# Performance work log

Measured on AMD Instinct MI355X. Metric: run time of the kernel, lower is better.

## Reference

```python
import jax, jax.numpy as jnp
import numpy as np
import math

EMBED = 512
HEADS = 2
HEAD_DIM = EMBED // HEADS
EPS = 1e-5

def layer_norm(x, g, b):
    mu = jnp.mean(x, axis=-1, keepdims=True)
    var = jnp.var(x, axis=-1, keepdims=True)
    return (x - mu) * jax.lax.rsqrt(var + EPS) * g + b

def setup_inputs() -> dict:
    key = jax.random.key(0)
    ks = jax.random.split(key, 16)
    s = 0.02
    inp = {
        "text_embeds": jax.random.normal(ks[0], (128, 32, EMBED), jnp.float32),
        "video_embeds": jax.random.normal(ks[1], (64, 12, EMBED), jnp.float32),
        "ln1_g": jnp.ones((EMBED,), jnp.float32),
        "ln1_b": jnp.zeros((EMBED,), jnp.float32),
        "Wq": jax.random.normal(ks[2], (EMBED, EMBED), jnp.float32) * s,
        "bq": jnp.zeros((EMBED,), jnp.float32),
        "Wk": jax.random.normal(ks[3], (EMBED, EMBED), jnp.float32) * s,
        "bk": jnp.zeros((EMBED,), jnp.float32),
        "Wv": jax.random.normal(ks[4], (EMBED, EMBED), jnp.float32) * s,
        "bv": jnp.zeros((EMBED,), jnp.float32),
        "Wo": jax.random.normal(ks[5], (EMBED, EMBED), jnp.float32) * s,
        "bo": jnp.zeros((EMBED,), jnp.float32),
        "Wl": jax.random.normal(ks[6], (EMBED, EMBED), jnp.float32) * s,
        "bl": jnp.zeros((EMBED,), jnp.float32),
        "ln2_g": jnp.ones((EMBED,), jnp.float32),
        "ln2_b": jnp.zeros((EMBED,), jnp.float32),
        "ln3_g": jnp.ones((EMBED,), jnp.float32),
        "ln3_b": jnp.zeros((EMBED,), jnp.float32),
    }
    return inp

def reference(text_embeds, video_embeds, ln1_g, ln1_b, Wq, bq, Wk, bk, Wv, bv,
              Wo, bo, Wl, bl, ln2_g, ln2_b, ln3_g, ln3_b):
    # shared layer_norm1 on both modalities
    t = layer_norm(text_embeds, ln1_g, ln1_b)    # [T, Nw, E]
    vd = layer_norm(video_embeds, ln1_g, ln1_b)  # [V, F, E]
    T, Nw, _ = t.shape
    V, Fr, _ = vd.shape
    q = (t @ Wq.T + bq).reshape(T, Nw, HEADS, HEAD_DIM)   # bthd
    k = (vd @ Wk.T + bk).reshape(V, Fr, HEADS, HEAD_DIM)  # avhd
    v = (vd @ Wv.T + bv).reshape(V, Fr, HEADS, HEAD_DIM)  # avhd
    # cross-modal outer-product attention logits: [V, T, H, F, Nw]
    logits = jnp.einsum('avhd,bthd->abhvt', k, q) / math.sqrt(HEAD_DIM)
    weights = jax.nn.softmax(logits, axis=3)  # softmax over frames
    attn = jnp.einsum('avhd,abhvt->abhtd', v, weights)  # [V, T, H, Nw, D]
    attn = attn.transpose(0, 1, 3, 2, 4).reshape(V, T, Nw, EMBED)
    attn = attn.mean(axis=0)                    # [T, Nw, E]
    o = attn @ Wo.T + bo
    o = layer_norm(o, ln2_g, ln2_b)
    lin = o @ Wl.T + bl  # dropout is identity in eval mode
    out = layer_norm(o + lin, ln3_g, ln3_b)
    return out
```

## Files before the change

kernel.cpp:

```cpp
#include <hip/hip_runtime.h>
#include <math.h>

#define EMBED 512
#define HD 256
#define FR 12
#define NV 64
#define NT_TOK 4096
#define NV_TOK 768

typedef __attribute__((ext_vector_type(8))) short short8;
typedef __attribute__((ext_vector_type(4))) float f32x4;

__device__ __forceinline__ unsigned int f2bf(float f) {
  unsigned int u = __float_as_uint(f);
  u += 0x7FFFu + ((u >> 16) & 1u);
  return u >> 16;
}
__device__ __forceinline__ void async_cp16(void* lds, const void* g) {
  __builtin_amdgcn_global_load_lds(
      (const __attribute__((address_space(1))) void*)g,
      (__attribute__((address_space(3))) void*)lds, 16, 0, 0);
}

__device__ __forceinline__ void gemm64_core(
    const unsigned short* __restrict__ Ab, int lda,
    const unsigned short* __restrict__ Bb, int ldb,
    int m0, int n0, int K,
    unsigned short* __restrict__ As, unsigned short* __restrict__ Bs,
    f32x4 acc[2][2]) {
  int tid = threadIdx.x;
  int w = tid >> 6, lane = tid & 63;
  int lr = lane & 15, quad = lane >> 4;
  int wm = (w >> 1) * 32, wn = (w & 1) * 32;
  int rowS[2], cgS[2];
  #pragma unroll
  for (int i = 0; i < 2; ++i) {
    int s = tid + i * 256;
    rowS[i] = s >> 3; cgS[i] = (s & 7) ^ (rowS[i] & 7);
  }
  int nk = K >> 6;
  #pragma unroll
  for (int i = 0; i < 2; ++i) {
    async_cp16(&As[(tid + i * 256) * 8],
               Ab + (size_t)(m0 + rowS[i]) * lda + cgS[i] * 8);
    async_cp16(&Bs[(tid + i * 256) * 8],
               Bb + (size_t)(n0 + rowS[i]) * ldb + cgS[i] * 8);
  }
  for (int k = 0; k < nk; ++k) {
    int cur = k & 1;
    __syncthreads();
    if (k + 1 < nk) {
      int nxt = cur ^ 1, koff = (k + 1) << 6;
      #pragma unroll
      for (int i = 0; i < 2; ++i) {
        async_cp16(&As[nxt * 4096 + (tid + i * 256) * 8],
                   Ab + (size_t)(m0 + rowS[i]) * lda + koff + cgS[i] * 8);
        async_cp16(&Bs[nxt * 4096 + (tid + i * 256) * 8],
                   Bb + (size_t)(n0 + rowS[i]) * ldb + koff + cgS[i] * 8);
      }
    }
    const unsigned short* Ac = As + cur * 4096;
    const unsigned short* Bc = Bs + cur * 4096;
    #pragma unroll
    for (int kk = 0; kk < 2; ++kk) {
      int sw = ((kk * 4 + quad) ^ (lr & 7)) * 8;
      short8 a0 = *(const short8*)&Ac[(wm + lr) * 64 + sw];
      short8 a1 = *(const short8*)&Ac[(wm + 16 + lr) * 64 + sw];
      short8 b0 = *(const short8*)&Bc[(wn + lr) * 64 + sw];
      short8 b1 = *(const short8*)&Bc[(wn + 16 + lr) * 64 + sw];
      acc[0][0] = __builtin_amdgcn_mfma_f32_16x16x32_bf16(a0, b0, acc[0][0], 0, 0, 0);
      acc[0][1] = __builtin_amdgcn_mfma_f32_16x16x32_bf16(a0, b1, acc[0][1], 0, 0, 0);
      acc[1][0] = __builtin_amdgcn_mfma_f32_16x16x32_bf16(a1, b0, acc[1][0], 0, 0, 0);
      acc[1][1] = __builtin_amdgcn_mfma_f32_16x16x32_bf16(a1, b1, acc[1][1], 0, 0, 0);
    }
  }
}

template <int MODE, bool BIAS>
__global__ __launch_bounds__(256, 4) void gemm64(
    const unsigned short* __restrict__ A, int lda, long AzS,
    const unsigned short* __restrict__ B, int ldb, long BzS,
    const float* __restrict__ bias, void* __restrict__ Cv, int ldc, long CzS,
    int K) {
  __shared__ __align__(16) unsigned short As[2 * 4096];
  __shared__ __align__(16) unsigned short Bs[2 * 4096];
  f32x4 acc[2][2] = {};
  const unsigned short* Ab = A + (size_t)blockIdx.z * AzS;
  const unsigned short* Bb = B + (size_t)blockIdx.z * BzS;
  int m0 = blockIdx.x * 64, n0 = blockIdx.y * 64;
  gemm64_core(Ab, lda, Bb, ldb, m0, n0, K, As, Bs, acc);
  int w = threadIdx.x >> 6, lane = threadIdx.x & 63;
  int lr = lane & 15, quad = lane >> 4;
  int wm = (w >> 1) * 32, wn = (w & 1) * 32;
  long cz = (long)blockIdx.z * CzS;
  #pragma unroll
  for (int j = 0; j < 2; ++j) {
    int col = n0 + wn + j * 16 + lr;
    float bv = BIAS ? bias[col] : 0.0f;
    #pragma unroll
    for (int i = 0; i < 2; ++i) {
      int rbase = m0 + wm + i * 16 + quad * 4;
      #pragma unroll
      for (int r = 0; r < 4; ++r) {
        float v = acc[i][j][r] + bv;
        if (MODE == 0)
          ((unsigned short*)Cv)[cz + (size_t)(rbase + r) * ldc + col] =
              (unsigned short)f2bf(v);
        else
          ((float*)Cv)[cz + (size_t)(rbase + r) * ldc + col] = v;
      }
    }
  }
}

__global__ __launch_bounds__(256, 4) void qkv_kernel(
    const unsigned short* __restrict__ tn, const unsigned short* __restrict__ vn,
    const unsigned short* __restrict__ Wq, const unsigned short* __restrict__ Wk,
    const unsigned short* __restrict__ Wv,
    const float* __restrict__ bq, const float* __restrict__ bk,
    const float* __restrict__ bv,
    unsigned short* __restrict__ Q, unsigned short* __restrict__ Kout,
    unsigned short* __restrict__ Vt) {
  __shared__ __align__(16) unsigned short As[2 * 4096];
  __shared__ __align__(16) unsigned short Bs[2 * 4096];
  int bid = blockIdx.x;
  const unsigned short *Ap, *Bp;
  const float* bias;
  unsigned short* outp = nullptr;
  int m0, n0, mode;
  if (bid < 512) {
    Ap = tn; Bp = Wq; bias = bq; outp = Q;
    m0 = (bid >> 3) * 64; n0 = (bid & 7) * 64; mode = 0;
  } else if (bid < 608) {
    int i = bid - 512;
    Ap = vn; Bp = Wk; bias = bk; outp = Kout;
    m0 = (i >> 3) * 64; n0 = (i & 7) * 64; mode = 0;
  } else {
    int i = bid - 608;
    Ap = vn; Bp = Wv; bias = bv;
    m0 = (i >> 3) * 64; n0 = (i & 7) * 64; mode = 1;
  }
  f32x4 acc[2][2] = {};
  gemm64_core(Ap, EMBED, Bp, EMBED, m0, n0, EMBED, As, Bs, acc);
  int w = threadIdx.x >> 6, lane = threadIdx.x & 63;
  int lr = lane & 15, quad = lane >> 4;
  int wm = (w >> 1) * 32, wn = (w & 1) * 32;
  #pragma unroll
  for (int j = 0; j < 2; ++j) {
    int col = n0 + wn + j * 16 + lr;
    float bvv = bias[col];
    #pragma unroll
    for (int i = 0; i < 2; ++i) {
      int rbase = m0 + wm + i * 16 + quad * 4;
      if (mode == 0) {
        #pragma unroll
        for (int r = 0; r < 4; ++r)
          outp[(size_t)(rbase + r) * EMBED + col] =
              (unsigned short)f2bf(acc[i][j][r] + bvv);
      } else {
        ushort4 pk;
        pk.x = (unsigned short)f2bf(acc[i][j][0] + bvv);
        pk.y = (unsigned short)f2bf(acc[i][j][1] + bvv);
        pk.z = (unsigned short)f2bf(acc[i][j][2] + bvv);
        pk.w = (unsigned short)f2bf(acc[i][j][3] + bvv);
        *(ushort4*)&Vt[(size_t)col * NV_TOK + rbase] = pk;
      }
    }
  }
}

__global__ __launch_bounds__(256, 4) void sgemm_softmax(
    const unsigned short* __restrict__ Q, const unsigned short* __restrict__ Kb,
    unsigned short* __restrict__ P) {
  __shared__ __align__(16) char smem[40960];
  unsigned short* As = (unsigned short*)smem;
  unsigned short* Bs = (unsigned short*)(smem + 16384);
  int tid = threadIdx.x;
  int w = tid >> 6, lane = tid & 63;
  int lr = lane & 15, quad = lane >> 4;
  int wm = (w >> 1) * 32, wn = (w & 1) * 48;
  int h = blockIdx.z;
  int m0 = blockIdx.x * 64, n0 = blockIdx.y * 96;
  const unsigned short* Ab = Q + h * HD;
  const unsigned short* Bb = Kb + h * HD;
  int rowA[2], cgA[2], rowB[3], cgB[3];
  #pragma unroll
  for (int i = 0; i < 2; ++i) {
    int s = tid + i * 256;
    rowA[i] = s >> 3; cgA[i] = (s & 7) ^ (rowA[i] & 7);
  }
  #pragma unroll
  for (int i = 0; i < 3; ++i) {
    int s = tid + i * 256;
    rowB[i] = s >> 3; cgB[i] = (s & 7) ^ (rowB[i] & 7);
  }
  f32x4 acc[2][3] = {};
  const int nk = HD >> 6;
  #pragma unroll
  for (int i = 0; i < 2; ++i)
    async_cp16(&As[(tid + i * 256) * 8],
               Ab + (size_t)(m0 + rowA[i]) * EMBED + cgA[i] * 8);
  #pragma unroll
  for (int i = 0; i < 3; ++i)
    async_cp16(&Bs[(tid + i * 256) * 8],
               Bb + (size_t)(n0 + rowB[i]) * EMBED + cgB[i] * 8);
  for (int k = 0; k < nk; ++k) {
    int cur = k & 1;
    __syncthreads();
    if (k + 1 < nk) {
      int nxt = cur ^ 1, koff = (k + 1) << 6;
      #pragma unroll
      for (int i = 0; i < 2; ++i)
        async_cp16(&As[nxt * 4096 + (tid + i * 256) * 8],
                   Ab + (size_t)(m0 + rowA[i]) * EMBED + koff + cgA[i] * 8);
      #pragma unroll
      for (int i = 0; i < 3; ++i)
        async_cp16(&Bs[nxt * 6144 + (tid + i * 256) * 8],
                   Bb + (size_t)(n0 + rowB[i]) * EMBED + koff + cgB[i] * 8);
    }
    const unsigned short* Ac = As + cur * 4096;
    const unsigned short* Bc = Bs + cur * 6144;
    #pragma unroll
    for (int kk = 0; kk < 2; ++kk) {
      int sw = ((kk * 4 + quad) ^ (lr & 7)) * 8;
      short8 a0 = *(const short8*)&Ac[(wm + lr) * 64 + sw];
      short8 a1 = *(const short8*)&Ac[(wm + 16 + lr) * 64 + sw];
      short8 b0 = *(const short8*)&Bc[(wn + lr) * 64 + sw];
      short8 b1 = *(const short8*)&Bc[(wn + 16 + lr) * 64 + sw];
      short8 b2 = *(const short8*)&Bc[(wn + 32 + lr) * 64 + sw];
      acc[0][0] = __builtin_amdgcn_mfma_f32_16x16x32_bf16(a0, b0, acc[0][0], 0, 0, 0);
      acc[0][1] = __builtin_amdgcn_mfma_f32_16x16x32_bf16(a0, b1, acc[0][1], 0, 0, 0);
      acc[0][2] = __builtin_amdgcn_mfma_f32_16x16x32_bf16(a0, b2, acc[0][2], 0, 0, 0);
      acc[1][0] = __builtin_amdgcn_mfma_f32_16x16x32_bf16(a1, b0, acc[1][0], 0, 0, 0);
      acc[1][1] = __builtin_amdgcn_mfma_f32_16x16x32_bf16(a1, b1, acc[1][1], 0, 0, 0);
      acc[1][2] = __builtin_amdgcn_mfma_f32_16x16x32_bf16(a1, b2, acc[1][2], 0, 0, 0);
    }
  }
  __syncthreads();
  float* Sx = (float*)smem;
  #pragma unroll
  for (int j = 0; j < 3; ++j) {
    int col = wn + j * 16 + lr;
    #pragma unroll
    for (int i = 0; i < 2; ++i) {
      int rbase = wm + i * 16 + quad * 4;
      #pragma unroll
      for (int r = 0; r < 4; ++r) Sx[(rbase + r) * 100 + col] = acc[i][j][r];
    }
  }
  __syncthreads();
  unsigned short* Ph = P + (size_t)h * NT_TOK * NV_TOK;
  #pragma unroll
  for (int gi = 0; gi < 2; ++gi) {
    int g = tid * 2 + gi;
    int row = g >> 3, gr = g & 7;
    const float* sp = Sx + row * 100 + gr * 12;
    float v[12];
    float m = -1e30f;
    #pragma unroll
    for (int f = 0; f < FR; ++f) { v[f] = sp[f] * 0.0625f; m = fmaxf(m, v[f]); }
    float s = 0.f;
    #pragma unroll
    for (int f = 0; f < FR; ++f) { v[f] = __expf(v[f] - m); s += v[f]; }
    float inv = (1.0f / NV) / s;
    unsigned short* pp = Ph + (size_t)(m0 + row) * NV_TOK + n0 + gr * 12;
    #pragma unroll
    for (int ii = 0; ii < 6; ++ii) {
      unsigned int lo = f2bf(v[2 * ii] * inv), hi = f2bf(v[2 * ii + 1] * inv);
      *(unsigned int*)(pp + 2 * ii) = lo | (hi << 16);
    }
  }
}

__device__ __forceinline__ void ln_row(
    const float* __restrict__ xr, const float* __restrict__ rr,
    const float* __restrict__ g, const float* __restrict__ b,
    float* __restrict__ outf, unsigned short* __restrict__ outb) {
  int t = threadIdx.x;
  float v0 = xr[t], v1 = xr[t + 256];
  if (rr != nullptr) { v0 += rr[t]; v1 += rr[t + 256]; }
  float s = v0 + v1;
  float s2 = v0 * v0 + v1 * v1;
  #pragma unroll
  for (int off = 32; off > 0; off >>= 1) {
    s += __shfl_down(s, off, 64);
    s2 += __shfl_down(s2, off, 64);
  }
  __shared__ float ss[4], ss2[4];
  __shared__ float mean_s, rstd_s;
  int wid = t >> 6;
  if ((t & 63) == 0) { ss[wid] = s; ss2[wid] = s2; }
  __syncthreads();
  if (t == 0) {
    float a = ss[0] + ss[1] + ss[2] + ss[3];
    float a2 = ss2[0] + ss2[1] + ss2[2] + ss2[3];
    float mean = a * (1.0f / EMBED);
    float var = a2 * (1.0f / EMBED) - mean * mean;
    mean_s = mean;
    rstd_s = rsqrtf(var + 1e-5f);
  }
  __syncthreads();
  float mean = mean_s, rstd = rstd_s;
  float y0 = (v0 - mean) * rstd * g[t] + b[t];
  float y1 = (v1 - mean) * rstd * g[t + 256] + b[t + 256];
  if (outf != nullptr) { outf[t] = y0; outf[t + 256] = y1; }
  if (outb != nullptr) {
    outb[t] = (unsigned short)f2bf(y0);
    outb[t + 256] = (unsigned short)f2bf(y1);
  }
}

__global__ __launch_bounds__(256) void ln_kernel(
    const float* __restrict__ x, const float* __restrict__ res,
    const float* __restrict__ g, const float* __restrict__ b,
    float* __restrict__ outf, unsigned short* __restrict__ outb) {
  size_t row = blockIdx.x;
  ln_row(x + row * EMBED, res ? res + row * EMBED : nullptr, g, b,
         outf ? outf + row * EMBED : nullptr,
         outb ? outb + row * EMBED : nullptr);
}

__global__ __launch_bounds__(256) void prep_kernel(
    const float* __restrict__ text, const float* __restrict__ video,
    const float* __restrict__ g, const float* __restrict__ b,
    const float* __restrict__ Wq, const float* __restrict__ Wk,
    const float* __restrict__ Wv, const float* __restrict__ Wo,
    const float* __restrict__ Wl, unsigned short* __restrict__ Wbf,
    unsigned short* __restrict__ tn, unsigned short* __restrict__ vn) {
  int bid = blockIdx.x;
  if (bid < 1280) {
    int i = bid * 256 + threadIdx.x;
    const float* srcs[5] = {Wq, Wk, Wv, Wo, Wl};
    const float* src = srcs[i >> 16];
    float4 v = ((const float4*)src)[i & 65535];
    uint2 o;
    o.x = f2bf(v.x) | (f2bf(v.y) << 16);
    o.y = f2bf(v.z) | (f2bf(v.w) << 16);
    ((uint2*)Wbf)[i] = o;
    return;
  }
  if (bid < 1280 + NT_TOK) {
    size_t row = bid - 1280;
    ln_row(text + row * EMBED, nullptr, g, b, nullptr, tn + row * EMBED);
  } else {
    size_t row = bid - (1280 + NT_TOK);
    ln_row(video + row * EMBED, nullptr, g, b, nullptr, vn + row * EMBED);
  }
}

extern "C" void kernel_launch(void* const* d_in, const int* in_sizes, int n_in,
                              void* d_out, int out_size, void* d_ws, size_t ws_size,
                              hipStream_t stream) {
  (void)in_sizes; (void)n_in; (void)out_size; (void)ws_size;
  const float* text  = (const float*)d_in[0];
  const float* video = (const float*)d_in[1];
  const float* ln1_g = (const float*)d_in[2];
  const float* ln1_b = (const float*)d_in[3];
  const float* Wq = (const float*)d_in[4];
  const float* bq = (const float*)d_in[5];
  const float* Wk = (const float*)d_in[6];
  const float* bk = (const float*)d_in[7];
  const float* Wv = (const float*)d_in[8];
  const float* bv = (const float*)d_in[9];
  const float* Wo = (const float*)d_in[10];
  const float* bo = (const float*)d_in[11];
  const float* Wl = (const float*)d_in[12];
  const float* bl = (const float*)d_in[13];
  const float* ln2_g = (const float*)d_in[14];
  const float* ln2_b = (const float*)d_in[15];
  const float* ln3_g = (const float*)d_in[16];
  const float* ln3_b = (const float*)d_in[17];
  float* out = (float*)d_out;

  char* base = (char*)d_ws;
  unsigned short* Wbf   = (unsigned short*)base;
  unsigned short* Wq_bf = Wbf + 0 * 262144;
  unsigned short* Wk_bf = Wbf + 1 * 262144;
  unsigned short* Wv_bf = Wbf + 2 * 262144;
  unsigned short* Wo_bf = Wbf + 3 * 262144;
  unsigned short* Wl_bf = Wbf + 4 * 262144;
  unsigned short* Vt    = (unsigned short*)(base + 2621440);
  char* big = base + 3407872;
  unsigned short* Q_bf  = (unsigned short*)(big + 0);
  unsigned short* K_bf  = (unsigned short*)(big + 4194304);
  unsigned short* P     = (unsigned short*)(big + 4980736);
  unsigned short* tn_bf = (unsigned short*)(big + 17563648);
  unsigned short* vn_bf = (unsigned short*)(big + 21757952);
  unsigned short* att_bf = tn_bf;
  float* Ob  = (float*)(big + 4980736);
  float* o2f = (float*)(big + 13369344);
  unsigned short* o2_bf = vn_bf;
  float* lin = (float*)(big + 0);

  prep_kernel<<<1280 + NT_TOK + NV_TOK, 256, 0, stream>>>(
      text, video, ln1_g, ln1_b, Wq, Wk, Wv, Wo, Wl, Wbf, tn_bf, vn_bf);

  qkv_kernel<<<704, 256, 0, stream>>>(tn_bf, vn_bf, Wq_bf, Wk_bf, Wv_bf,
                                      bq, bk, bv, Q_bf, K_bf, Vt);

  sgemm_softmax<<<dim3(64, 8, 2), 256, 0, stream>>>(Q_bf, K_bf, P);

  gemm64<0, false><<<dim3(64, 4, 2), 256, 0, stream>>>(
      P, NV_TOK, (long)NT_TOK * NV_TOK, Vt, NV_TOK, (long)HD * NV_TOK, nullptr,
      att_bf, EMBED, HD, NV_TOK);

  gemm64<1, true><<<dim3(64, 8, 1), 256, 0, stream>>>(
      att_bf, EMBED, 0, Wo_bf, EMBED, 0, bo, Ob, EMBED, 0, EMBED);
  ln_kernel<<<NT_TOK, 256, 0, stream>>>(Ob, nullptr, ln2_g, ln2_b, o2f, o2_bf);
  gemm64<1, true><<<dim3(64, 8, 1), 256, 0, stream>>>(
      o2_bf, EMBED, 0, Wl_bf, EMBED, 0, bl, lin, EMBED, 0, EMBED);
  ln_kernel<<<NT_TOK, 256, 0, stream>>>(o2f, lin, ln3_g, ln3_b, out, nullptr);
}
```

Baseline: 162.7 us.

## Fold Wo into V to merge attention-V and output projection GEMMs

Precomputes W2 = Wo_h · V_h^T per head (a 512x1536 matrix) inside the softmax kernel as extra blocks. The output projection then becomes a single GEMM of P [4096x1536] with W2, with K=1536. This removes the separate P·V GEMM launch, the att_bf intermediate and the transposed V layout. The combined product rounds W2 to bf16, which changes numerics slightly, and the final GEMM runs over a longer K than before.

Measured after the change: 164.2 us. About the same (+0.9%).

```diff
diff --git a/kernel.cpp b/kernel.cpp
--- a/kernel.cpp
+++ b/kernel.cpp
@@ -120,25 +120,25 @@
     const float* __restrict__ bq, const float* __restrict__ bk,
     const float* __restrict__ bv,
     unsigned short* __restrict__ Q, unsigned short* __restrict__ Kout,
-    unsigned short* __restrict__ Vt) {
+    unsigned short* __restrict__ V) {
   __shared__ __align__(16) unsigned short As[2 * 4096];
   __shared__ __align__(16) unsigned short Bs[2 * 4096];
   int bid = blockIdx.x;
   const unsigned short *Ap, *Bp;
   const float* bias;
-  unsigned short* outp = nullptr;
-  int m0, n0, mode;
+  unsigned short* outp;
+  int m0, n0;
   if (bid < 512) {
     Ap = tn; Bp = Wq; bias = bq; outp = Q;
-    m0 = (bid >> 3) * 64; n0 = (bid & 7) * 64; mode = 0;
+    m0 = (bid >> 3) * 64; n0 = (bid & 7) * 64;
   } else if (bid < 608) {
     int i = bid - 512;
     Ap = vn; Bp = Wk; bias = bk; outp = Kout;
-    m0 = (i >> 3) * 64; n0 = (i & 7) * 64; mode = 0;
+    m0 = (i >> 3) * 64; n0 = (i & 7) * 64;
   } else {
     int i = bid - 608;
-    Ap = vn; Bp = Wv; bias = bv;
-    m0 = (i >> 3) * 64; n0 = (i & 7) * 64; mode = 1;
+    Ap = vn; Bp = Wv; bias = bv; outp = V;
+    m0 = (i >> 3) * 64; n0 = (i & 7) * 64;
   }
   f32x4 acc[2][2] = {};
   gemm64_core(Ap, EMBED, Bp, EMBED, m0, n0, EMBED, As, Bs, acc);
@@ -152,35 +152,53 @@
     #pragma unroll
     for (int i = 0; i < 2; ++i) {
       int rbase = m0 + wm + i * 16 + quad * 4;
-      if (mode == 0) {
-        #pragma unroll
-        for (int r = 0; r < 4; ++r)
-          outp[(size_t)(rbase + r) * EMBED + col] =
-              (unsigned short)f2bf(acc[i][j][r] + bvv);
-      } else {
-        ushort4 pk;
-        pk.x = (unsigned short)f2bf(acc[i][j][0] + bvv);
-        pk.y = (unsigned short)f2bf(acc[i][j][1] + bvv);
-        pk.z = (unsigned short)f2bf(acc[i][j][2] + bvv);
-        pk.w = (unsigned short)f2bf(acc[i][j][3] + bvv);
-        *(ushort4*)&Vt[(size_t)col * NV_TOK + rbase] = pk;
-      }
+      #pragma unroll
+      for (int r = 0; r < 4; ++r)
+        outp[(size_t)(rbase + r) * EMBED + col] =
+            (unsigned short)f2bf(acc[i][j][r] + bvv);
     }
   }
 }
 
 __global__ __launch_bounds__(256, 4) void sgemm_softmax(
     const unsigned short* __restrict__ Q, const unsigned short* __restrict__ Kb,
-    unsigned short* __restrict__ P) {
+    const unsigned short* __restrict__ V, const unsigned short* __restrict__ Wo,
+    unsigned short* __restrict__ P, unsigned short* __restrict__ W2) {
   __shared__ __align__(16) char smem[40960];
-  unsigned short* As = (unsigned short*)smem;
-  unsigned short* Bs = (unsigned short*)(smem + 16384);
   int tid = threadIdx.x;
   int w = tid >> 6, lane = tid & 63;
   int lr = lane & 15, quad = lane >> 4;
+  int bid = blockIdx.x;
+
+  if (bid >= 1024) {
+    int j = bid - 1024;
+    int h = j / 96, i = j % 96;
+    int m0 = (i / 12) * 64, n0 = (i % 12) * 64;
+    unsigned short* As = (unsigned short*)smem;
+    unsigned short* Bs = (unsigned short*)(smem + 16384);
+    f32x4 acc[2][2] = {};
+    gemm64_core(Wo + h * HD, EMBED, V + h * HD, EMBED, m0, n0, HD, As, Bs, acc);
+    int wm = (w >> 1) * 32, wn = (w & 1) * 32;
+    #pragma unroll
+    for (int j2 = 0; j2 < 2; ++j2) {
+      int col = n0 + wn + j2 * 16 + lr;
+      #pragma unroll
+      for (int i2 = 0; i2 < 2; ++i2) {
+        int rbase = m0 + wm + i2 * 16 + quad * 4;
+        #pragma unroll
+        for (int r = 0; r < 4; ++r)
+          W2[(size_t)(rbase + r) * 1536 + h * 768 + col] =
+              (unsigned short)f2bf(acc[i2][j2][r]);
+      }
+    }
+    return;
+  }
+
+  unsigned short* As = (unsigned short*)smem;
+  unsigned short* Bs = (unsigned short*)(smem + 16384);
   int wm = (w >> 1) * 32, wn = (w & 1) * 48;
-  int h = blockIdx.z;
-  int m0 = blockIdx.x * 64, n0 = blockIdx.y * 96;
+  int h = bid >> 9, rem = bid & 511;
+  int m0 = (rem >> 3) * 64, n0 = (rem & 7) * 96;
   const unsigned short* Ab = Q + h * HD;
   const unsigned short* Bb = Kb + h * HD;
   int rowA[2], cgA[2], rowB[3], cgB[3];
@@ -249,7 +267,6 @@
     }
   }
   __syncthreads();
-  unsigned short* Ph = P + (size_t)h * NT_TOK * NV_TOK;
   #pragma unroll
   for (int gi = 0; gi < 2; ++gi) {
     int g = tid * 2 + gi;
@@ -263,7 +280,8 @@
     #pragma unroll
     for (int f = 0; f < FR; ++f) { v[f] = __expf(v[f] - m); s += v[f]; }
     float inv = (1.0f / NV) / s;
-    unsigned short* pp = Ph + (size_t)(m0 + row) * NV_TOK + n0 + gr * 12;
+    unsigned short* pp =
+        P + (size_t)(m0 + row) * 1536 + h * 768 + n0 + gr * 12;
     #pragma unroll
     for (int ii = 0; ii < 6; ++ii) {
       unsigned int lo = f2bf(v[2 * ii] * inv), hi = f2bf(v[2 * ii + 1] * inv);
@@ -379,33 +397,29 @@
   unsigned short* Wv_bf = Wbf + 2 * 262144;
   unsigned short* Wo_bf = Wbf + 3 * 262144;
   unsigned short* Wl_bf = Wbf + 4 * 262144;
-  unsigned short* Vt    = (unsigned short*)(base + 2621440);
-  char* big = base + 3407872;
-  unsigned short* Q_bf  = (unsigned short*)(big + 0);
-  unsigned short* K_bf  = (unsigned short*)(big + 4194304);
-  unsigned short* P     = (unsigned short*)(big + 4980736);
-  unsigned short* tn_bf = (unsigned short*)(big + 17563648);
-  unsigned short* vn_bf = (unsigned short*)(big + 21757952);
-  unsigned short* att_bf = tn_bf;
-  float* Ob  = (float*)(big + 4980736);
-  float* o2f = (float*)(big + 13369344);
-  unsigned short* o2_bf = vn_bf;
-  float* lin = (float*)(big + 0);
+  unsigned short* W2    = (unsigned short*)(base + 2621440);
+  unsigned short* tn_bf = (unsigned short*)(base + 4194304);
+  unsigned short* vn_bf = (unsigned short*)(base + 8388608);
+  unsigned short* Q_bf  = (unsigned short*)(base + 9175040);
+  unsigned short* K_bf  = (unsigned short*)(base + 13369344);
+  unsigned short* V_bf  = (unsigned short*)(base + 14155776);
+  unsigned short* P     = (unsigned short*)(base + 14942208);
+  float* Ob  = (float*)(base + 4194304);
+  float* o2f = (float*)(base + 14942208);
+  unsigned short* o2_bf = (unsigned short*)(base + 23330816);
+  float* lin = (float*)(base + 4194304);
 
   prep_kernel<<<1280 + NT_TOK + NV_TOK, 256, 0, stream>>>(
       text, video, ln1_g, ln1_b, Wq, Wk, Wv, Wo, Wl, Wbf, tn_bf, vn_bf);
 
   qkv_kernel<<<704, 256, 0, stream>>>(tn_bf, vn_bf, Wq_bf, Wk_bf, Wv_bf,
-                                      bq, bk, bv, Q_bf, K_bf, Vt);
-
-  sgemm_softmax<<<dim3(64, 8, 2), 256, 0, stream>>>(Q_bf, K_bf, P);
-
-  gemm64<0, false><<<dim3(64, 4, 2), 256, 0, stream>>>(
-      P, NV_TOK, (long)NT_TOK * NV_TOK, Vt, NV_TOK, (long)HD * NV_TOK, nullptr,
-      att_bf, EMBED, HD, NV_TOK);
+                                      bq, bk, bv, Q_bf, K_bf, V_bf);
+
+  sgemm_softmax<<<1216, 256, 0, stream>>>(Q_bf, K_bf, V_bf, Wo_bf, P, W2);
 
   gemm64<1, true><<<dim3(64, 8, 1), 256, 0, stream>>>(
-      att_bf, EMBED, 0, Wo_bf, EMBED, 0, bo, Ob, EMBED, 0, EMBED);
+      P, 1536, 0, W2, 1536, 0, bo, Ob, EMBED, 0, 1536);
+
   ln_kernel<<<NT_TOK, 256, 0, stream>>>(Ob, nullptr, ln2_g, ln2_b, o2f, o2_bf);
   gemm64<1, true><<<dim3(64, 8, 1), 256, 0, stream>>>(
       o2_bf, EMBED, 0, Wl_bf, EMBED, 0, bl, lin, EMBED, 0, EMBED);
```
